# Kernel tuning notes

Measured on AMD Instinct MI355X. Metric: run time of the kernel, lower is better.

## Reference

```python
import jax, jax.numpy as jnp
import numpy as np

B, S, DIM, NUM_BANDS = 8, 32768, 128, 64
MAX_FREQ = 10000.0


def setup_inputs() -> dict:
    key = jax.random.key(0)
    k1, k2, k3 = jax.random.split(key, 3)
    x = jax.random.normal(k1, (B, S, DIM), dtype=jnp.float32)
    positions = jnp.arange(B * S, dtype=jnp.int64 if jax.config.x64_enabled else jnp.int32).reshape(B, S) % S
    # log-spaced frequency bands as in the torch init
    frequency_bands = jnp.exp(jnp.linspace(jnp.log(1.0), jnp.log(MAX_FREQ), NUM_BANDS)).astype(jnp.float32)
    phase_shifts = jnp.zeros((NUM_BANDS,), dtype=jnp.float32)
    attn_w = jax.random.normal(k2, (NUM_BANDS, DIM), dtype=jnp.float32) * (1.0 / np.sqrt(DIM))
    attn_b = jnp.zeros((NUM_BANDS,), dtype=jnp.float32)
    return {
        "x": x,
        "positions": positions,
        "frequency_bands": frequency_bands,
        "phase_shifts": phase_shifts,
        "attn_w": attn_w,
        "attn_b": attn_b,
    }


def reference(x, positions, frequency_bands, phase_shifts, attn_w, attn_b):
    b, s, dim = x.shape
    num_bands = frequency_bands.shape[0]
    pos = positions.astype(x.dtype)  # [B,S]
    # all bands at once: angle [B,S,num_bands]
    angle = pos[..., None] * frequency_bands + phase_shifts
    # interleave sin/cos per band: layout [sin0,cos0,sin1,cos1,...] == dim
    enc = jnp.stack([jnp.sin(angle), jnp.cos(angle)], axis=-1).reshape(b, s, dim)
    # adaptive frequency attention: Linear(dim->num_bands) + softmax
    freq_attn = jax.nn.softmax(jnp.einsum("bsd,nd->bsn", x, attn_w) + attn_b, axis=-1)
    # each band weight applies to its sin and cos components
    attn = jnp.repeat(freq_attn, 2, axis=-1)  # [B,S,dim]
    return x + enc * attn
```

## Files before the change

kernel.cpp:

```cpp
#include <hip/hip_runtime.h>
#include <hip/hip_bf16.h>


#define NTOK  (8 * 32768)
#define NTILE (NTOK / 16)
#define WPB   4
#define NBLK  (NTILE / WPB)

typedef short  bf16x8 __attribute__((ext_vector_type(8)));
typedef float  f32x4  __attribute__((ext_vector_type(4)));

static __device__ __forceinline__ short f2bf(float f) {
    __hip_bfloat16 h = __float2bfloat16(f);
    return __builtin_bit_cast(short, h);
}

__global__ __launch_bounds__(256, 3) void afpe_r11(
    const float* __restrict__ x, const int* __restrict__ pos,
    const float* __restrict__ fb, const float* __restrict__ ph,
    const float* __restrict__ aw, const float* __restrict__ ab,
    float* __restrict__ out)
{
    __shared__ __align__(16) char wlds[16384];
    __shared__ __align__(16) char sbuf[4][8192];
    __shared__ float pfb[64], pph[64], pab[64];

    const int tid  = threadIdx.x;
    const int lane = tid & 63;
    const int wv   = tid >> 6;
    const int q    = lane >> 4;
    const int tt   = lane & 15;

    #pragma unroll
    for (int g0 = 0; g0 < 4; ++g0) {
        const int g  = g0 * 256 + tid;
        const int mc = g >> 6, l = g & 63;
        const int sm = mc >> 2, sc = mc & 3, sq = l >> 4, st = l & 15;
        const float* wp = aw + (size_t)(16 * sm + st) * 128 + sq * 8 + 32 * sc;
        const float4 w0 = *(const float4*)wp;
        const float4 w1 = *(const float4*)(wp + 4);
        bf16x8 a;
        a[0] = f2bf(w0.x); a[1] = f2bf(w0.y); a[2] = f2bf(w0.z); a[3] = f2bf(w0.w);
        a[4] = f2bf(w1.x); a[5] = f2bf(w1.y); a[6] = f2bf(w1.z); a[7] = f2bf(w1.w);
        *(bf16x8*)(wlds + mc * 1024 + l * 16) = a;
    }
    if (tid < 64) { pfb[tid] = fb[tid]; pph[tid] = ph[tid]; pab[tid] = ab[tid]; }
    __syncthreads();

    const int tile = blockIdx.x * WPB + wv;
    const char* xtile = (const char*)(x + (size_t)tile * 2048);
    char* sb = sbuf[wv];

    #pragma unroll
    for (int j = 0; j < 8; ++j) {
        const int g = 64 * j + lane;
        const int t = g >> 5;
        const int u = (g & 31) ^ (t & 7);
        __builtin_amdgcn_global_load_lds(
            (const __attribute__((address_space(1))) void*)(xtile + t * 512 + u * 16),
            (__attribute__((address_space(3))) void*)(sb + j * 1024),
            16, 0, 0);
    }
    const int p = pos[tile * 16 + tt];
    asm volatile("s_waitcnt vmcnt(0)" ::: "memory");

    float4 xf[8];
    #pragma unroll
    for (int c = 0; c < 4; ++c) {
        #pragma unroll
        for (int h = 0; h < 2; ++h) {
            const int u = 2 * q + 8 * c + h;
            xf[2 * c + h] = *(const float4*)(sb + tt * 512 + (u ^ (tt & 7)) * 16);
        }
    }

    f32x4 acc[4];
    #pragma unroll
    for (int m = 0; m < 4; ++m) {
        const float4 abv = *(const float4*)&pab[16 * m + 4 * q];
        acc[m][0] = abv.x; acc[m][1] = abv.y; acc[m][2] = abv.z; acc[m][3] = abv.w;
    }
    #pragma unroll
    for (int c = 0; c < 4; ++c) {
        const float4 b0 = xf[2 * c], b1 = xf[2 * c + 1];
        bf16x8 B;
        B[0] = f2bf(b0.x); B[1] = f2bf(b0.y); B[2] = f2bf(b0.z); B[3] = f2bf(b0.w);
        B[4] = f2bf(b1.x); B[5] = f2bf(b1.y); B[6] = f2bf(b1.z); B[7] = f2bf(b1.w);
        #pragma unroll
        for (int m = 0; m < 4; ++m) {
            const bf16x8 A = *(const bf16x8*)(wlds + (m * 4 + c) * 1024 + lane * 16);
            acc[m] = __builtin_amdgcn_mfma_f32_16x16x32_bf16(A, B, acc[m], 0, 0, 0);
        }
    }

    float e[4][4];
    float s = 0.f;
    #pragma unroll
    for (int m = 0; m < 4; ++m) {
        #pragma unroll
        for (int r = 0; r < 4; ++r) { e[m][r] = __expf(acc[m][r]); s += e[m][r]; }
    }
    s += __shfl_xor(s, 16, 64);
    s += __shfl_xor(s, 32, 64);
    const float rinv = 1.0f / s;

    const float pf = (float)p;
    #pragma unroll
    for (int c = 0; c < 4; ++c) {
        const float4 fq4 = *(const float4*)&pfb[16 * c + 4 * q];
        const float4 ph4 = *(const float4*)&pph[16 * c + 4 * q];
        const float fq[4] = {fq4.x, fq4.y, fq4.z, fq4.w};
        const float pq[4] = {ph4.x, ph4.y, ph4.z, ph4.w};
        float sa[4], ca[4];
        #pragma unroll
        for (int r = 0; r < 4; ++r) {
            float ang = pf * fq[r];
            ang = ang + pq[r];
            double td = (double)ang * 0.15915494309189535;
            td -= floor(td);
            const float rev = (float)td;
            const float at  = e[c][r] * rinv;
            sa[r] = __builtin_amdgcn_sinf(rev) * at;
            ca[r] = __builtin_amdgcn_cosf(rev) * at;
        }
        const float4 xv0 = xf[2 * c], xv1 = xf[2 * c + 1];
        f32x4 o0, o1;
        o0[0] = xv0.x + sa[0]; o0[1] = xv0.y + ca[0];
        o0[2] = xv0.z + sa[1]; o0[3] = xv0.w + ca[1];
        o1[0] = xv1.x + sa[2]; o1[1] = xv1.y + ca[2];
        o1[2] = xv1.z + sa[3]; o1[3] = xv1.w + ca[3];
        const int u0 = 2 * q + 8 * c;
        *(f32x4*)(sb + tt * 512 + ((u0)     ^ (tt & 7)) * 16) = o0;
        *(f32x4*)(sb + tt * 512 + ((u0 + 1) ^ (tt & 7)) * 16) = o1;
    }

    float* ob = out + (size_t)tile * 2048;
    #pragma unroll
    for (int j = 0; j < 8; ++j) {
        const int g  = 64 * j + lane;
        const int t  = g >> 5;
        const int up = g & 31;
        const f32x4 v = *(const f32x4*)(sb + t * 512 + (up ^ (t & 7)) * 16);
        *(f32x4*)(ob + t * 128 + up * 4) = v;
    }
}

extern "C" void kernel_launch(void* const* d_in, const int* in_sizes, int n_in,
                              void* d_out, int out_size, void* d_ws, size_t ws_size,
                              hipStream_t stream) {
    const float* x   = (const float*)d_in[0];
    const int*   pos = (const int*)d_in[1];
    const float* fb  = (const float*)d_in[2];
    const float* ph  = (const float*)d_in[3];
    const float* aw  = (const float*)d_in[4];
    const float* ab  = (const float*)d_in[5];
    float* out = (float*)d_out;

    afpe_r11<<<NBLK, 256, 0, stream>>>(x, pos, fb, ph, aw, ab, out);
}
```

Baseline: 48.63 us.

## Process four tiles per wave with overlapped next-tile staging

Each wave now handles four consecutive 16-token tiles instead of one, which cuts the grid by a factor of four and spreads the per-block weight conversion to LDS over more work. After computing a tile, the output is pulled into registers and the next tile's global-to-LDS load is issued before the current tile's global stores. A partial vmcnt wait then lets the stores stay in flight while the next load completes. The costs are higher register pressure from holding the output in registers and fewer blocks, which may leave CUs underfilled or reduce latency hiding.

```diff
diff --git a/kernel.cpp b/kernel.cpp
--- a/kernel.cpp
+++ b/kernel.cpp
@@ -5,7 +5,8 @@
 #define NTOK  (8 * 32768)
 #define NTILE (NTOK / 16)
 #define WPB   4
-#define NBLK  (NTILE / WPB)
+#define TPW   4
+#define NBLK  (NTILE / (WPB * TPW))
 
 typedef short  bf16x8 __attribute__((ext_vector_type(8)));
 typedef float  f32x4  __attribute__((ext_vector_type(4)));
@@ -15,7 +16,21 @@
     return __builtin_bit_cast(short, h);
 }
 
-__global__ __launch_bounds__(256, 3) void afpe_r11(
+static __device__ __forceinline__ void stage_tile(const char* __restrict__ xtile,
+                                                  char* sb, int lane) {
+    #pragma unroll
+    for (int j = 0; j < 8; ++j) {
+        const int g = 64 * j + lane;
+        const int t = g >> 5;
+        const int u = (g & 31) ^ (t & 7);
+        __builtin_amdgcn_global_load_lds(
+            (const __attribute__((address_space(1))) void*)(xtile + t * 512 + u * 16),
+            (__attribute__((address_space(3))) void*)(sb + j * 1024),
+            16, 0, 0);
+    }
+}
+
+__global__ __launch_bounds__(256, 3) void afpe_r12(
     const float* __restrict__ x, const int* __restrict__ pos,
     const float* __restrict__ fb, const float* __restrict__ ph,
     const float* __restrict__ aw, const float* __restrict__ ab,
@@ -47,101 +62,116 @@
     if (tid < 64) { pfb[tid] = fb[tid]; pph[tid] = ph[tid]; pab[tid] = ab[tid]; }
     __syncthreads();
 
-    const int tile = blockIdx.x * WPB + wv;
-    const char* xtile = (const char*)(x + (size_t)tile * 2048);
+    const int tbase = (blockIdx.x * WPB + wv) * TPW;
     char* sb = sbuf[wv];
 
+    int pv[TPW];
     #pragma unroll
-    for (int j = 0; j < 8; ++j) {
-        const int g = 64 * j + lane;
-        const int t = g >> 5;
-        const int u = (g & 31) ^ (t & 7);
-        __builtin_amdgcn_global_load_lds(
-            (const __attribute__((address_space(1))) void*)(xtile + t * 512 + u * 16),
-            (__attribute__((address_space(3))) void*)(sb + j * 1024),
-            16, 0, 0);
-    }
-    const int p = pos[tile * 16 + tt];
+    for (int s = 0; s < TPW; ++s) pv[s] = pos[(tbase + s) * 16 + tt];
+    stage_tile((const char*)(x + (size_t)tbase * 2048), sb, lane);
     asm volatile("s_waitcnt vmcnt(0)" ::: "memory");
 
-    float4 xf[8];
     #pragma unroll
-    for (int c = 0; c < 4; ++c) {
+    for (int it = 0; it < TPW; ++it) {
+        const int tile = tbase + it;
+
+        float4 xf[8];
         #pragma unroll
-        for (int h = 0; h < 2; ++h) {
-            const int u = 2 * q + 8 * c + h;
-            xf[2 * c + h] = *(const float4*)(sb + tt * 512 + (u ^ (tt & 7)) * 16);
+        for (int c = 0; c < 4; ++c) {
+            #pragma unroll
+            for (int h = 0; h < 2; ++h) {
+                const int u = 2 * q + 8 * c + h;
+                xf[2 * c + h] = *(const float4*)(sb + tt * 512 + (u ^ (tt & 7)) * 16);
+            }
         }
-    }
 
-    f32x4 acc[4];
-    #pragma unroll
-    for (int m = 0; m < 4; ++m) {
-        const float4 abv = *(const float4*)&pab[16 * m + 4 * q];
-        acc[m][0] = abv.x; acc[m][1] = abv.y; acc[m][2] = abv.z; acc[m][3] = abv.w;
-    }
-    #pragma unroll
-    for (int c = 0; c < 4; ++c) {
-        const float4 b0 = xf[2 * c], b1 = xf[2 * c + 1];
-        bf16x8 B;
-        B[0] = f2bf(b0.x); B[1] = f2bf(b0.y); B[2] = f2bf(b0.z); B[3] = f2bf(b0.w);
-        B[4] = f2bf(b1.x); B[5] = f2bf(b1.y); B[6] = f2bf(b1.z); B[7] = f2bf(b1.w);
+        f32x4 acc[4];
         #pragma unroll
         for (int m = 0; m < 4; ++m) {
-            const bf16x8 A = *(const bf16x8*)(wlds + (m * 4 + c) * 1024 + lane * 16);
-            acc[m] = __builtin_amdgcn_mfma_f32_16x16x32_bf16(A, B, acc[m], 0, 0, 0);
+            const float4 abv = *(const float4*)&pab[16 * m + 4 * q];
+            acc[m][0] = abv.x; acc[m][1] = abv.y; acc[m][2] = abv.z; acc[m][3] = abv.w;
         }
-    }
+        #pragma unroll
+        for (int c = 0; c < 4; ++c) {
+            const float4 b0 = xf[2 * c], b1 = xf[2 * c + 1];
+            bf16x8 B;
+            B[0] = f2bf(b0.x); B[1] = f2bf(b0.y); B[2] = f2bf(b0.z); B[3] = f2bf(b0.w);
+            B[4] = f2bf(b1.x); B[5] = f2bf(b1.y); B[6] = f2bf(b1.z); B[7] = f2bf(b1.w);
+            #pragma unroll
+            for (int m = 0; m < 4; ++m) {
+                const bf16x8 A = *(const bf16x8*)(wlds + (m * 4 + c) * 1024 + lane * 16);
+                acc[m] = __builtin_amdgcn_mfma_f32_16x16x32_bf16(A, B, acc[m], 0, 0, 0);
+            }
+        }
 
-    float e[4][4];
-    float s = 0.f;
-    #pragma unroll
-    for (int m = 0; m < 4; ++m) {
+        float e[4][4];
+        float s = 0.f;
         #pragma unroll
-        for (int r = 0; r < 4; ++r) { e[m][r] = __expf(acc[m][r]); s += e[m][r]; }
-    }
-    s += __shfl_xor(s, 16, 64);
-    s += __shfl_xor(s, 32, 64);
-    const float rinv = 1.0f / s;
+        for (int m = 0; m < 4; ++m) {
+            #pragma unroll
+            for (int r = 0; r < 4; ++r) { e[m][r] = __expf(acc[m][r]); s += e[m][r]; }
+        }
+        s += __shfl_xor(s, 16, 64);
+        s += __shfl_xor(s, 32, 64);
+        const float rinv = 1.0f / s;
 
-    const float pf = (float)p;
-    #pragma unroll
-    for (int c = 0; c < 4; ++c) {
-        const float4 fq4 = *(const float4*)&pfb[16 * c + 4 * q];
-        const float4 ph4 = *(const float4*)&pph[16 * c + 4 * q];
-        const float fq[4] = {fq4.x, fq4.y, fq4.z, fq4.w};
-        const float pq[4] = {ph4.x, ph4.y, ph4.z, ph4.w};
-        float sa[4], ca[4];
+        const float pf = (float)pv[it];
         #pragma unroll
-        for (int r = 0; r < 4; ++r) {
-            float ang = pf * fq[r];
-            ang = ang + pq[r];
-            double td = (double)ang * 0.15915494309189535;
-            td -= floor(td);
-            const float rev = (float)td;
-            const float at  = e[c][r] * rinv;
-            sa[r] = __builtin_amdgcn_sinf(rev) * at;
-            ca[r] = __builtin_amdgcn_cosf(rev) * at;
+        for (int c = 0; c < 4; ++c) {
+            const float4 fq4 = *(const float4*)&pfb[16 * c + 4 * q];
+            const float4 ph4 = *(const float4*)&pph[16 * c + 4 * q];
+            const float fq[4] = {fq4.x, fq4.y, fq4.z, fq4.w};
+            const float pq[4] = {ph4.x, ph4.y, ph4.z, ph4.w};
+            float sa[4], ca[4];
+            #pragma unroll
+            for (int r = 0; r < 4; ++r) {
+                float ang = pf * fq[r];
+                ang = ang + pq[r];
+                double td = (double)ang * 0.15915494309189535;
+                td -= floor(td);
+                const float rev = (float)td;
+                const float at  = e[c][r] * rinv;
+                sa[r] = __builtin_amdgcn_sinf(rev) * at;
+                ca[r] = __builtin_amdgcn_cosf(rev) * at;
+            }
+            const float4 xv0 = xf[2 * c], xv1 = xf[2 * c + 1];
+            f32x4 o0, o1;
+            o0[0] = xv0.x + sa[0]; o0[1] = xv0.y + ca[0];
+            o0[2] = xv0.z + sa[1]; o0[3] = xv0.w + ca[1];
+            o1[0] = xv1.x + sa[2]; o1[1] = xv1.y + ca[2];
+            o1[2] = xv1.z + sa[3]; o1[3] = xv1.w + ca[3];
+            const int u0 = 2 * q + 8 * c;
+            *(f32x4*)(sb + tt * 512 + ((u0)     ^ (tt & 7)) * 16) = o0;
+            *(f32x4*)(sb + tt * 512 + ((u0 + 1) ^ (tt & 7)) * 16) = o1;
         }
-        const float4 xv0 = xf[2 * c], xv1 = xf[2 * c + 1];
-        f32x4 o0, o1;
-        o0[0] = xv0.x + sa[0]; o0[1] = xv0.y + ca[0];
-        o0[2] = xv0.z + sa[1]; o0[3] = xv0.w + ca[1];
-        o1[0] = xv1.x + sa[2]; o1[1] = xv1.y + ca[2];
-        o1[2] = xv1.z + sa[3]; o1[3] = xv1.w + ca[3];
-        const int u0 = 2 * q + 8 * c;
-        *(f32x4*)(sb + tt * 512 + ((u0)     ^ (tt & 7)) * 16) = o0;
-        *(f32x4*)(sb + tt * 512 + ((u0 + 1) ^ (tt & 7)) * 16) = o1;
-    }
 
-    float* ob = out + (size_t)tile * 2048;
-    #pragma unroll
-    for (int j = 0; j < 8; ++j) {
-        const int g  = 64 * j + lane;
-        const int t  = g >> 5;
-        const int up = g & 31;
-        const f32x4 v = *(const f32x4*)(sb + t * 512 + (up ^ (t & 7)) * 16);
-        *(f32x4*)(ob + t * 128 + up * 4) = v;
+        f32x4 vout[8];
+        #pragma unroll
+        for (int j = 0; j < 8; ++j) {
+            const int g  = 64 * j + lane;
+            const int t  = g >> 5;
+            const int up = g & 31;
+            vout[j] = *(const f32x4*)(sb + t * 512 + (up ^ (t & 7)) * 16);
+        }
+        asm volatile("s_waitcnt lgkmcnt(0)" ::: "memory");
+        __builtin_amdgcn_sched_barrier(0);
+
+        if (it < TPW - 1)
+            stage_tile((const char*)(x + (size_t)(tile + 1) * 2048), sb, lane);
+        __builtin_amdgcn_sched_barrier(0);
+
+        float* ob = out + (size_t)tile * 2048;
+        #pragma unroll
+        for (int j = 0; j < 8; ++j) {
+            const int g  = 64 * j + lane;
+            const int t  = g >> 5;
+            const int up = g & 31;
+            *(f32x4*)(ob + t * 128 + up * 4) = vout[j];
+        }
+        __builtin_amdgcn_sched_barrier(0);
+
+        if (it < TPW - 1)
+            asm volatile("s_waitcnt vmcnt(8)" ::: "memory");
     }
 }
 
@@ -156,5 +186,5 @@
     const float* ab  = (const float*)d_in[5];
     float* out = (float*)d_out;
 
-    afpe_r11<<<NBLK, 256, 0, stream>>>(x, pos, fb, ph, aw, ab, out);
+    afpe_r12<<<NBLK, 256, 0, stream>>>(x, pos, fb, ph, aw, ab, out);
 }
```

New measurement: 72.00 us. 48.0% more time.
